# Optimization experiments

Measured on AMD Instinct MI355X. Metric: run time of the kernel, lower is better.

Reference implementation:

```python
import jax, jax.numpy as jnp
import numpy as np

P = 16          # patch size (square)
HEADS = 8
DH = 64         # dim per head
SCALE = DH ** -0.5
EPS = 1e-5


def layernorm(x, g, b):
    mu = x.mean(-1, keepdims=True)
    var = ((x - mu) ** 2).mean(-1, keepdims=True)
    return (x - mu) * jax.lax.rsqrt(var + EPS) * g + b


def sattn(q, k, v):
    # q:[..., i, d], k/v:[..., j, d]; q already scaled
    sim = jnp.einsum('...id,...jd->...ij', q, k)
    a = jax.nn.softmax(sim, axis=-1)
    return jnp.einsum('...ij,...jd->...id', a, v)


def split_heads(t, b, N):
    return t.reshape(b, N, HEADS, DH).transpose(0, 2, 1, 3).reshape(b * HEADS, N, DH)


def merge_heads(t, b, N):
    return t.reshape(b, HEADS, N, DH).transpose(0, 2, 1, 3).reshape(b, N, HEADS * DH)


def qkv_cls(x, ln_g, ln_b, qkv_w):
    b, N, _ = x.shape
    xn = layernorm(x, ln_g, ln_b)
    q, k, v = jnp.split(xn @ qkv_w, 3, axis=-1)
    q = split_heads(q, b, N) * SCALE
    k = split_heads(k, b, N)
    v = split_heads(v, b, N)
    cls_out = sattn(q[:, :1], k, v)          # cls attends to everything
    return q[:, 1:], k[:, 1:], v[:, 1:], k[:, :1], v[:, :1], cls_out


def time_attention(x, ln_g, ln_b, qkv_w, out_w, out_b, f, n):
    b, N, _ = x.shape
    q_, k_, v_, cls_k, cls_v, cls_out = qkv_cls(x, ln_g, ln_b, qkv_w)
    bh = b * HEADS
    resh = lambda t: t.reshape(bh, f, n, DH).transpose(0, 2, 1, 3)  # 'b (f n) d -> (b n) f d' kept as [bh,n,f,d]
    q_, k_, v_ = resh(q_), resh(k_), resh(v_)
    ck = jnp.broadcast_to(cls_k[:, None], (bh, n, 1, DH))
    cv = jnp.broadcast_to(cls_v[:, None], (bh, n, 1, DH))
    out = sattn(q_, jnp.concatenate([ck, k_], 2), jnp.concatenate([cv, v_], 2))
    out = out.transpose(0, 2, 1, 3).reshape(bh, f * n, DH)
    out = jnp.concatenate([cls_out, out], axis=1)
    return merge_heads(out, b, N) @ out_w + out_b


def space_attention(x, ln_g, ln_b, qkv_w, out_w, out_b, f, n):
    b, N, _ = x.shape
    q_, k_, v_, cls_k, cls_v, cls_out = qkv_cls(x, ln_g, ln_b, qkv_w)
    bh = b * HEADS
    resh = lambda t: t.reshape(bh, f, n, DH)  # 'b (f n) d -> (b f) n d' kept as [bh,f,n,d]
    q_, k_, v_ = resh(q_), resh(k_), resh(v_)
    m = n // 2
    ck = jnp.broadcast_to(cls_k[:, None], (bh, f, 1, DH))
    cv = jnp.broadcast_to(cls_v[:, None], (bh, f, 1, DH))
    # mutual attention: first half queries attend to [cls, second half], and vice versa
    out1 = sattn(q_[:, :, :m], jnp.concatenate([ck, k_[:, :, m:]], 2), jnp.concatenate([cv, v_[:, :, m:]], 2))
    out2 = sattn(q_[:, :, m:], jnp.concatenate([ck, k_[:, :, :m]], 2), jnp.concatenate([cv, v_[:, :, :m]], 2))
    out = jnp.concatenate([out1, out2], axis=2).reshape(bh, f * n, DH)
    out = jnp.concatenate([cls_out, out], axis=1)
    return merge_heads(out, b, N) @ out_w + out_b


def geglu_ff(x, ln_g, ln_b, w1, b1, w2, b2):
    xn = layernorm(x, ln_g, ln_b)
    h = xn @ w1 + b1
    u, g = jnp.split(h, 2, axis=-1)
    return (u * jax.nn.gelu(g, approximate=False)) @ w2 + b2


def setup_inputs() -> dict:
    key = jax.random.key(0)
    ks = jax.random.split(key, 12)
    D, DEPTH, NC = 512, 12, 60
    inner = HEADS * DH
    B, F, C, H, W = 1, 4, 3, 480, 640
    n = (H // P) * (W // P)        # 1200
    N = F * n + 1                  # 4801
    pd = C * P * P                 # 768
    s = 0.02
    rn = lambda k, sh: jax.random.normal(k, sh, jnp.float32) * s
    z = lambda sh: jnp.zeros(sh, jnp.float32)
    o = lambda sh: jnp.ones(sh, jnp.float32)
    return {
        'video': jax.random.normal(ks[0], (B, F, C, H, W), jnp.float32),
        'patch_w': rn(ks[1], (pd, D)), 'patch_b': z((D,)),
        'pos_emb': rn(ks[2], (N, D)),
        'cls_token': rn(ks[3], (1, D)),
        't_ln_g': o((DEPTH, D)), 't_ln_b': z((DEPTH, D)),
        't_qkv_w': rn(ks[4], (DEPTH, D, 3 * inner)),
        't_out_w': rn(ks[5], (DEPTH, inner, D)), 't_out_b': z((DEPTH, D)),
        's_ln_g': o((DEPTH, D)), 's_ln_b': z((DEPTH, D)),
        's_qkv_w': rn(ks[6], (DEPTH, D, 3 * inner)),
        's_out_w': rn(ks[7], (DEPTH, inner, D)), 's_out_b': z((DEPTH, D)),
        'f_ln_g': o((DEPTH, D)), 'f_ln_b': z((DEPTH, D)),
        'f_w1': rn(ks[8], (DEPTH, D, 8 * D)), 'f_b1': z((DEPTH, 8 * D)),
        'f_w2': rn(ks[9], (DEPTH, 4 * D, D)), 'f_b2': z((DEPTH, D)),
        'o_ln_g': o((D,)), 'o_ln_b': z((D,)),
        'o_w': rn(ks[10], (D, NC)), 'o_b': z((NC,)),
    }


def reference(video, patch_w, patch_b, pos_emb, cls_token,
              t_ln_g, t_ln_b, t_qkv_w, t_out_w, t_out_b,
              s_ln_g, s_ln_b, s_qkv_w, s_out_w, s_out_b,
              f_ln_g, f_ln_b, f_w1, f_b1, f_w2, f_b2,
              o_ln_g, o_ln_b, o_w, o_b):
    b, f, c, H, W = video.shape
    hh, ww = H // P, W // P
    n = hh * ww
    wh = ww // 2
    half = W // 2

    def patchify(v):  # v: [b,f,c,H,W/2] -> [b, f*hh*wh, P*P*c]
        v = v.reshape(b, f, c, hh, P, wh, P)
        v = v.transpose(0, 1, 3, 5, 4, 6, 2)  # b f h w p1 p2 c
        return v.reshape(b, f * hh * wh, P * P * c)

    tok = jnp.concatenate([patchify(video[..., :half]), patchify(video[..., half:])], axis=1)
    tok = tok @ patch_w + patch_b
    x = jnp.concatenate([jnp.broadcast_to(cls_token[None], (b, 1, tok.shape[-1])), tok], axis=1)
    x = x + pos_emb[: x.shape[1]]

    depth = t_qkv_w.shape[0]
    for i in range(depth):
        x = time_attention(x, t_ln_g[i], t_ln_b[i], t_qkv_w[i], t_out_w[i], t_out_b[i], f, n) + x
        x = space_attention(x, s_ln_g[i], s_ln_b[i], s_qkv_w[i], s_out_w[i], s_out_b[i], f, n) + x
        x = geglu_ff(x, f_ln_g[i], f_ln_b[i], f_w1[i], f_b1[i], f_w2[i], f_b2[i]) + x

    cls = layernorm(x[:, 0], o_ln_g, o_ln_b)
    return cls @ o_w + o_b
```

## Files before the change

kernel.cpp:

```cpp
#include <hip/hip_runtime.h>
#include <cmath>


#define NT      4801
#define NP      4800
#define MP      4864
#define DM      512
#define QKV_ST  1536
#define LN_EPS  1e-5f
#define NCH     49

typedef __attribute__((ext_vector_type(8))) short bf16x8;
typedef __attribute__((ext_vector_type(4))) float f32x4;

__device__ __forceinline__ unsigned short f2b(float f) {
    union { float f; unsigned int u; } x; x.f = f;
    unsigned int r = (x.u + 0x7FFFu + ((x.u >> 16) & 1u)) >> 16;
    return (unsigned short)r;
}
__device__ __forceinline__ float b2f(unsigned short b) {
    union { unsigned int u; float f; } x; x.u = ((unsigned int)b) << 16;
    return x.f;
}
__device__ __forceinline__ unsigned int pack2(float a, float b) {
    return (unsigned int)f2b(a) | ((unsigned int)f2b(b) << 16);
}

__device__ __forceinline__ void gl_lds16(const void* g, void* l) {
    __builtin_amdgcn_global_load_lds(
        (__attribute__((address_space(1))) unsigned int*)(unsigned long long)(uintptr_t)g,
        (__attribute__((address_space(3))) unsigned int*)l, 16, 0, 0);
}

__global__ void patchify_kernel(const float* __restrict__ video, unsigned short* __restrict__ out)
{
    int idx = blockIdx.x * 256 + threadIdx.x;
    if (idx >= NP * 768) return;
    int tok = idx / 768, e = idx % 768;
    int c  = e % 3;
    int pe = e / 3;
    int p2 = pe % 16, p1 = pe / 16;
    int half = tok / 2400, r = tok % 2400;
    int f = r / 600, rr = r % 600;
    int hi = rr / 20, wi = rr % 20;
    int row = hi * 16 + p1;
    int col = half * 320 + wi * 16 + p2;
    out[idx] = f2b(video[(((size_t)f * 3 + c) * 480 + row) * 640 + col]);
}

__global__ void cls_init_kernel(const float* __restrict__ cls_token,
                                const float* __restrict__ pos, float* __restrict__ X)
{
    int d = blockIdx.x * 256 + threadIdx.x;
    if (d < DM) X[d] = cls_token[d] + pos[d];
}

__device__ __forceinline__ void transpose_tile(const float* __restrict__ in,
                                               unsigned short* __restrict__ out,
                                               int K, int N, int tile)
{
    __shared__ float T[32][33];
    int ntk = K / 32;
    int kt = tile % ntk, nt = tile / ntk;
    int k0 = kt * 32, n0 = nt * 32;
    int tx = threadIdx.x & 31, ty = threadIdx.x >> 5;
    #pragma unroll
    for (int i = 0; i < 4; i++)
        T[ty + 8 * i][tx] = in[(size_t)(k0 + ty + 8 * i) * N + n0 + tx];
    __syncthreads();
    #pragma unroll
    for (int i = 0; i < 4; i++)
        out[(size_t)(n0 + ty + 8 * i) * K + k0 + tx] = f2b(T[tx][ty + 8 * i]);
}

__global__ __launch_bounds__(256) void convertT_layer(
    const float* __restrict__ w0, const float* __restrict__ w1,
    const float* __restrict__ w2, const float* __restrict__ w3,
    const float* __restrict__ w4, const float* __restrict__ w5,
    unsigned short* __restrict__ out)
{
    int t = blockIdx.x;
    if      (t <  768) transpose_tile(w0, out + 0,       512, 1536, t);
    else if (t < 1024) transpose_tile(w1, out + 786432,  512,  512, t - 768);
    else if (t < 1792) transpose_tile(w2, out + 1048576, 512, 1536, t - 1024);
    else if (t < 2048) transpose_tile(w3, out + 1835008, 512,  512, t - 1792);
    else if (t < 4096) transpose_tile(w4, out + 2097152, 512, 4096, t - 2048);
    else               transpose_tile(w5, out + 4194304, 2048, 512, t - 4096);
}

__global__ __launch_bounds__(256) void convertT_one(
    const float* __restrict__ in, unsigned short* __restrict__ out, int K, int N)
{
    transpose_tile(in, out, K, N, blockIdx.x);
}

template<bool OB16>
__global__ __launch_bounds__(256, 2) void mfma_gemm(
    const unsigned short* __restrict__ A, const unsigned short* __restrict__ BT,
    const float* __restrict__ bias, const float* __restrict__ add,
    void* __restrict__ C, int Mv, int N, int K)
{
    __shared__ short Asm[2][128 * 64];
    __shared__ short Bsm[2][128 * 64];
    const int tid = threadIdx.x, w = tid >> 6, lane = tid & 63;
    const int row0 = blockIdx.y * 128, col0 = blockIdx.x * 128;
    const int wm = w >> 1, wn = w & 1;
    const int l15 = lane & 15, quad = lane >> 4;

    f32x4 acc[4][4] = {};

    int arows[4], aqs[4];
    #pragma unroll
    for (int i = 0; i < 4; i++) {
        int s = (w * 4 + i) * 64 + lane;
        arows[i] = s >> 3;
        aqs[i]   = (s & 7) ^ ((s >> 3) & 7);
    }
    const unsigned short* Ab = A  + (size_t)row0 * K;
    const unsigned short* Bb = BT + (size_t)col0 * K;

    #pragma unroll
    for (int i = 0; i < 4; i++) {
        gl_lds16(Ab + (size_t)arows[i] * K + aqs[i] * 8, &Asm[0][(w * 4 + i) * 512]);
        gl_lds16(Bb + (size_t)arows[i] * K + aqs[i] * 8, &Bsm[0][(w * 4 + i) * 512]);
    }
    asm volatile("s_waitcnt vmcnt(0)" ::: "memory");
    __builtin_amdgcn_s_barrier();

    const int nt = K >> 6;
    int cur = 0;
    for (int t = 0; t < nt; t++) {
        if (t + 1 < nt) {
            const int k0 = (t + 1) << 6;
            #pragma unroll
            for (int i = 0; i < 4; i++) {
                gl_lds16(Ab + (size_t)arows[i] * K + k0 + aqs[i] * 8,
                         &Asm[cur ^ 1][(w * 4 + i) * 512]);
                gl_lds16(Bb + (size_t)arows[i] * K + k0 + aqs[i] * 8,
                         &Bsm[cur ^ 1][(w * 4 + i) * 512]);
            }
        }
        __builtin_amdgcn_sched_barrier(0);
        const short* As = Asm[cur];
        const short* Bs = Bsm[cur];
        #pragma unroll
        for (int ks = 0; ks < 2; ks++) {
            bf16x8 af[4], bfr[4];
            #pragma unroll
            for (int i = 0; i < 4; i++) {
                int m  = wm * 64 + i * 16 + l15;
                int pa = (ks * 4 + quad) ^ (m & 7);
                af[i]  = *(const bf16x8*)&As[m * 64 + pa * 8];
                int n  = wn * 64 + i * 16 + l15;
                int pb = (ks * 4 + quad) ^ (n & 7);
                bfr[i] = *(const bf16x8*)&Bs[n * 64 + pb * 8];
            }
            #pragma unroll
            for (int i = 0; i < 4; i++)
                #pragma unroll
                for (int j = 0; j < 4; j++)
                    acc[i][j] = __builtin_amdgcn_mfma_f32_16x16x32_bf16(
                                    af[i], bfr[j], acc[i][j], 0, 0, 0);
        }
        asm volatile("s_waitcnt vmcnt(0)" ::: "memory");
        __builtin_amdgcn_s_barrier();
        cur ^= 1;
    }

    #pragma unroll
    for (int i = 0; i < 4; i++) {
        #pragma unroll
        for (int r = 0; r < 4; r++) {
            int row = row0 + wm * 64 + i * 16 + quad * 4 + r;
            if (row >= Mv) continue;
            #pragma unroll
            for (int j = 0; j < 4; j++) {
                int col = col0 + wn * 64 + j * 16 + l15;
                float v = acc[i][j][r];
                if (bias) v += bias[col];
                if (add)  v += add[(size_t)row * N + col];
                if (OB16) ((unsigned short*)C)[(size_t)row * N + col] = f2b(v);
                else      ((float*)C)[(size_t)row * N + col] = v;
            }
        }
    }
}

template<int SPLITS>
__global__ __launch_bounds__(256, 2) void mfma_gemm_sk(
    const unsigned short* __restrict__ A, const unsigned short* __restrict__ BT,
    const float* __restrict__ bias, float* __restrict__ C, int Mv, int N, int K)
{
    __shared__ short Asm[2][128 * 64];
    __shared__ short Bsm[2][128 * 64];
    const int tid = threadIdx.x, w = tid >> 6, lane = tid & 63;
    const int row0 = blockIdx.y * 128, col0 = blockIdx.x * 128;
    const int wm = w >> 1, wn = w & 1;
    const int l15 = lane & 15, quad = lane >> 4;
    const int kchunk = K / SPLITS;
    const int kbeg = blockIdx.z * kchunk;

    f32x4 acc[4][4] = {};

    int arows[4], aqs[4];
    #pragma unroll
    for (int i = 0; i < 4; i++) {
        int s = (w * 4 + i) * 64 + lane;
        arows[i] = s >> 3;
        aqs[i]   = (s & 7) ^ ((s >> 3) & 7);
    }
    const unsigned short* Ab = A  + (size_t)row0 * K + kbeg;
    const unsigned short* Bb = BT + (size_t)col0 * K + kbeg;

    #pragma unroll
    for (int i = 0; i < 4; i++) {
        gl_lds16(Ab + (size_t)arows[i] * K + aqs[i] * 8, &Asm[0][(w * 4 + i) * 512]);
        gl_lds16(Bb + (size_t)arows[i] * K + aqs[i] * 8, &Bsm[0][(w * 4 + i) * 512]);
    }
    asm volatile("s_waitcnt vmcnt(0)" ::: "memory");
    __builtin_amdgcn_s_barrier();

    const int nt = kchunk >> 6;
    int cur = 0;
    for (int t = 0; t < nt; t++) {
        if (t + 1 < nt) {
            const int k0 = (t + 1) << 6;
            #pragma unroll
            for (int i = 0; i < 4; i++) {
                gl_lds16(Ab + (size_t)arows[i] * K + k0 + aqs[i] * 8,
                         &Asm[cur ^ 1][(w * 4 + i) * 512]);
                gl_lds16(Bb + (size_t)arows[i] * K + k0 + aqs[i] * 8,
                         &Bsm[cur ^ 1][(w * 4 + i) * 512]);
            }
        }
        __builtin_amdgcn_sched_barrier(0);
        const short* As = Asm[cur];
        const short* Bs = Bsm[cur];
        #pragma unroll
        for (int ks = 0; ks < 2; ks++) {
            bf16x8 af[4], bfr[4];
            #pragma unroll
            for (int i = 0; i < 4; i++) {
                int m  = wm * 64 + i * 16 + l15;
                int pa = (ks * 4 + quad) ^ (m & 7);
                af[i]  = *(const bf16x8*)&As[m * 64 + pa * 8];
                int n  = wn * 64 + i * 16 + l15;
                int pb = (ks * 4 + quad) ^ (n & 7);
                bfr[i] = *(const bf16x8*)&Bs[n * 64 + pb * 8];
            }
            #pragma unroll
            for (int i = 0; i < 4; i++)
                #pragma unroll
                for (int j = 0; j < 4; j++)
                    acc[i][j] = __builtin_amdgcn_mfma_f32_16x16x32_bf16(
                                    af[i], bfr[j], acc[i][j], 0, 0, 0);
        }
        asm volatile("s_waitcnt vmcnt(0)" ::: "memory");
        __builtin_amdgcn_s_barrier();
        cur ^= 1;
    }

    const bool addb = (blockIdx.z == 0) && (bias != nullptr);
    #pragma unroll
    for (int i = 0; i < 4; i++) {
        #pragma unroll
        for (int r = 0; r < 4; r++) {
            int row = row0 + wm * 64 + i * 16 + quad * 4 + r;
            if (row >= Mv) continue;
            #pragma unroll
            for (int j = 0; j < 4; j++) {
                int col = col0 + wn * 64 + j * 16 + l15;
                float v = acc[i][j][r];
                if (addb) v += bias[col];
                unsafeAtomicAdd(&C[(size_t)row * N + col], v);
            }
        }
    }
}

__global__ __launch_bounds__(256) void ln_bf16(
    const float* __restrict__ x, const float* __restrict__ g,
    const float* __restrict__ b, unsigned short* __restrict__ y, int M)
{
    int wid = threadIdx.x >> 6, lane = threadIdx.x & 63;
    int row = blockIdx.x * 4 + wid;
    if (row >= M) return;
    const float4* xr = (const float4*)(x + (size_t)row * DM);
    float4 v0 = xr[lane * 2], v1 = xr[lane * 2 + 1];
    float s  = v0.x + v0.y + v0.z + v0.w + v1.x + v1.y + v1.z + v1.w;
    float s2 = v0.x*v0.x + v0.y*v0.y + v0.z*v0.z + v0.w*v0.w
             + v1.x*v1.x + v1.y*v1.y + v1.z*v1.z + v1.w*v1.w;
    #pragma unroll
    for (int off = 32; off >= 1; off >>= 1) {
        s  += __shfl_xor(s, off);
        s2 += __shfl_xor(s2, off);
    }
    float mu = s * (1.f / DM);
    float var = s2 * (1.f / DM) - mu * mu;
    float r = rsqrtf(var + LN_EPS);
    const float4* gv = (const float4*)g;
    const float4* bv = (const float4*)b;
    unsigned int* yr = (unsigned int*)(y + (size_t)row * DM);
    #pragma unroll
    for (int i = 0; i < 2; i++) {
        float4 v = (i == 0) ? v0 : v1;
        float4 gg = gv[lane * 2 + i], bb = bv[lane * 2 + i];
        float ox = (v.x - mu) * r * gg.x + bb.x;
        float oy = (v.y - mu) * r * gg.y + bb.y;
        float oz = (v.z - mu) * r * gg.z + bb.z;
        float ow = (v.w - mu) * r * gg.w + bb.w;
        yr[lane * 4 + i * 2 + 0] = pack2(ox, oy);
        yr[lane * 4 + i * 2 + 1] = pack2(oz, ow);
    }
}

__global__ __launch_bounds__(256, 2) void time_attn(
    const unsigned short* __restrict__ qkv, unsigned short* __restrict__ out)
{
    int t = blockIdx.x * 256 + threadIdx.x;
    if (t >= 8 * NP) return;
    int h = t / NP, j = t - h * NP;
    int pos = j % 1200;
    union { bf16x8 v; unsigned short u[8]; } ld;
    float q[64];
    const unsigned short* qp = qkv + (size_t)(j + 1) * QKV_ST + h * 64;
    #pragma unroll
    for (int c = 0; c < 8; c++) {
        ld.v = *(const bf16x8*)(qp + c * 8);
        #pragma unroll
        for (int e = 0; e < 8; e++) q[c * 8 + e] = b2f(ld.u[e]) * 0.125f;
    }
    int rows[5] = {0, pos + 1, pos + 1201, pos + 2401, pos + 3601};
    float s[5];
    #pragma unroll
    for (int kk = 0; kk < 5; kk++) {
        const unsigned short* kp = qkv + (size_t)rows[kk] * QKV_ST + 512 + h * 64;
        float ss = 0.f;
        #pragma unroll
        for (int c = 0; c < 8; c++) {
            ld.v = *(const bf16x8*)(kp + c * 8);
            #pragma unroll
            for (int e = 0; e < 8; e++) ss += q[c * 8 + e] * b2f(ld.u[e]);
        }
        s[kk] = ss;
    }
    float mx = s[0];
    #pragma unroll
    for (int kk = 1; kk < 5; kk++) mx = fmaxf(mx, s[kk]);
    float e5[5], l = 0.f;
    #pragma unroll
    for (int kk = 0; kk < 5; kk++) { e5[kk] = __expf(s[kk] - mx); l += e5[kk]; }
    float rl = 1.f / l;
    float acc[64];
    #pragma unroll
    for (int d = 0; d < 64; d++) acc[d] = 0.f;
    #pragma unroll
    for (int kk = 0; kk < 5; kk++) {
        float p = e5[kk] * rl;
        const unsigned short* vp = qkv + (size_t)rows[kk] * QKV_ST + 1024 + h * 64;
        #pragma unroll
        for (int c = 0; c < 8; c++) {
            ld.v = *(const bf16x8*)(vp + c * 8);
            #pragma unroll
            for (int e = 0; e < 8; e++) acc[c * 8 + e] += p * b2f(ld.u[e]);
        }
    }
    unsigned int* op = (unsigned int*)(out + (size_t)(j + 1) * DM + h * 64);
    #pragma unroll
    for (int d2 = 0; d2 < 32; d2++) op[d2] = pack2(acc[2 * d2], acc[2 * d2 + 1]);
}

#define SPAD 72
__global__ __launch_bounds__(256, 2) void space_attn_mfma(
    const unsigned short* __restrict__ qkv, unsigned short* __restrict__ out)
{
    __shared__ short Ksm[64 * SPAD];
    __shared__ short VTsm[64 * SPAD];
    __shared__ short Psm[4][32 * SPAD];
    int qt = blockIdx.x, h = blockIdx.y, g = blockIdx.z;
    int f = g >> 1, half = g & 1;
    int tid = threadIdx.x, w = tid >> 6, lane = tid & 63;
    int l15 = lane & 15, quad = lane >> 4;

    int qrow_base = qt * 128 + w * 32;
    int qb = 1 + f * 1200 + half * 600;
    int kb = 1 + f * 1200 + (1 - half) * 600;

    bf16x8 aQ[2][2];
    #pragma unroll
    for (int mf = 0; mf < 2; mf++) {
        int qr = qrow_base + mf * 16 + l15;
        int qtok = qb + ((qr < 600) ? qr : 0);
        const unsigned short* qp = qkv + (size_t)qtok * QKV_ST + h * 64;
        #pragma unroll
        for (int ks = 0; ks < 2; ks++)
            aQ[mf][ks] = *(const bf16x8*)(qp + ks * 32 + quad * 8);
    }

    f32x4 O[2][4] = {};
    float mrow[2][4], lrow[2][4];
    #pragma unroll
    for (int mf = 0; mf < 2; mf++)
        #pragma unroll
        for (int r = 0; r < 4; r++) { mrow[mf][r] = -1e30f; lrow[mf][r] = 0.f; }

    for (int kt = 0; kt < 10; kt++) {
        __syncthreads();
        #pragma unroll
        for (int it = 0; it < 2; it++) {
            int c = tid + it * 256;
            int row = c >> 3, dc = (c & 7) * 8;
            int kidx = kt * 64 + row;
            int tok = (kidx == 0) ? 0 : ((kidx <= 600) ? kb + kidx - 1 : 0);
            const unsigned short* kp = qkv + (size_t)tok * QKV_ST + 512 + h * 64 + dc;
            *(bf16x8*)&Ksm[row * SPAD + dc] = *(const bf16x8*)kp;
            union { bf16x8 v; unsigned short u[8]; } vv;
            vv.v = *(const bf16x8*)(kp + 512);
            #pragma unroll
            for (int e = 0; e < 8; e++)
                VTsm[(dc + e) * SPAD + row] = vv.u[e];
        }
        __syncthreads();

        f32x4 S[2][4] = {};
        #pragma unroll
        for (int ks = 0; ks < 2; ks++) {
            bf16x8 bK[4];
            #pragma unroll
            for (int nf = 0; nf < 4; nf++)
                bK[nf] = *(const bf16x8*)&Ksm[(nf * 16 + l15) * SPAD + ks * 32 + quad * 8];
            #pragma unroll
            for (int mf = 0; mf < 2; mf++)
                #pragma unroll
                for (int nf = 0; nf < 4; nf++)
                    S[mf][nf] = __builtin_amdgcn_mfma_f32_16x16x32_bf16(
                                    aQ[mf][ks], bK[nf], S[mf][nf], 0, 0, 0);
        }

        #pragma unroll
        for (int mf = 0; mf < 2; mf++) {
            float pv[4][4];
            float lm[4] = {-1e30f, -1e30f, -1e30f, -1e30f};
            #pragma unroll
            for (int nf = 0; nf < 4; nf++) {
                int kidx = kt * 64 + nf * 16 + l15;
                bool valid = kidx <= 600;
                #pragma unroll
                for (int r = 0; r < 4; r++) {
                    float s = valid ? S[mf][nf][r] * 0.125f : -1e30f;
                    pv[nf][r] = s;
                    lm[r] = fmaxf(lm[r], s);
                }
            }
            #pragma unroll
            for (int off = 1; off < 16; off <<= 1)
                #pragma unroll
                for (int r = 0; r < 4; r++)
                    lm[r] = fmaxf(lm[r], __shfl_xor(lm[r], off));
            #pragma unroll
            for (int r = 0; r < 4; r++) {
                float nm = fmaxf(mrow[mf][r], lm[r]);
                float c = __expf(mrow[mf][r] - nm);
                mrow[mf][r] = nm;
                lrow[mf][r] *= c;
                #pragma unroll
                for (int nf = 0; nf < 4; nf++) O[mf][nf][r] *= c;
            }
            float rs[4] = {0.f, 0.f, 0.f, 0.f};
            #pragma unroll
            for (int nf = 0; nf < 4; nf++)
                #pragma unroll
                for (int r = 0; r < 4; r++) {
                    float p = __expf(pv[nf][r] - mrow[mf][r]);
                    pv[nf][r] = p;
                    rs[r] += p;
                }
            #pragma unroll
            for (int off = 1; off < 16; off <<= 1)
                #pragma unroll
                for (int r = 0; r < 4; r++)
                    rs[r] += __shfl_xor(rs[r], off);
            #pragma unroll
            for (int r = 0; r < 4; r++) lrow[mf][r] += rs[r];
            #pragma unroll
            for (int nf = 0; nf < 4; nf++)
                #pragma unroll
                for (int r = 0; r < 4; r++)
                    Psm[w][(mf * 16 + quad * 4 + r) * SPAD + nf * 16 + l15] = (short)f2b(pv[nf][r]);
        }
        asm volatile("s_waitcnt lgkmcnt(0)" ::: "memory");

        #pragma unroll
        for (int ks2 = 0; ks2 < 2; ks2++) {
            bf16x8 aP[2], bV[4];
            #pragma unroll
            for (int mf = 0; mf < 2; mf++)
                aP[mf] = *(const bf16x8*)&Psm[w][(mf * 16 + l15) * SPAD + ks2 * 32 + quad * 8];
            #pragma unroll
            for (int nf = 0; nf < 4; nf++)
                bV[nf] = *(const bf16x8*)&VTsm[(nf * 16 + l15) * SPAD + ks2 * 32 + quad * 8];
            #pragma unroll
            for (int mf = 0; mf < 2; mf++)
                #pragma unroll
                for (int nf = 0; nf < 4; nf++)
                    O[mf][nf] = __builtin_amdgcn_mfma_f32_16x16x32_bf16(
                                    aP[mf], bV[nf], O[mf][nf], 0, 0, 0);
        }
    }

    #pragma unroll
    for (int mf = 0; mf < 2; mf++)
        #pragma unroll
        for (int r = 0; r < 4; r++) {
            int qr = qrow_base + mf * 16 + quad * 4 + r;
            if (qr >= 600) continue;
            int qtok = qb + qr;
            float rl = 1.f / lrow[mf][r];
            #pragma unroll
            for (int nf = 0; nf < 4; nf++)
                out[(size_t)qtok * DM + h * 64 + nf * 16 + l15] = f2b(O[mf][nf][r] * rl);
        }
}

__global__ __launch_bounds__(256) void cls_attn_part(
    const unsigned short* __restrict__ qkv, float* __restrict__ part)
{
    int ch = blockIdx.x, h = blockIdx.y;
    int wid = threadIdx.x >> 6, lane = threadIdx.x & 63;
    __shared__ float sm[4], sl[4], sa[4][64];
    float qv = b2f(qkv[h * 64 + lane]) * 0.125f;
    int k0 = ch * 100 + wid * 25;
    float m = -1e30f, l = 0.f, acc = 0.f;
    for (int i = 0; i < 25; i += 2) {
        int key0 = k0 + i, key1 = key0 + 1;
        bool ok0 = key0 < NT;
        bool ok1 = (i + 1 < 25) && (key1 < NT);
        const unsigned short* kr0 = qkv + (size_t)(ok0 ? key0 : 0) * QKV_ST + 512 + h * 64;
        const unsigned short* kr1 = qkv + (size_t)(ok1 ? key1 : 0) * QKV_ST + 512 + h * 64;
        float s0 = qv * b2f(kr0[lane]);
        float v0 = b2f(kr0[512 + lane]);
        float s1 = qv * b2f(kr1[lane]);
        float v1 = b2f(kr1[512 + lane]);
        #pragma unroll
        for (int off = 32; off >= 1; off >>= 1) {
            s0 += __shfl_xor(s0, off);
            s1 += __shfl_xor(s1, off);
        }
        float nm = m;
        if (ok0) nm = fmaxf(nm, s0);
        if (ok1) nm = fmaxf(nm, s1);
        float c  = __expf(m - nm);
        float p0 = ok0 ? __expf(s0 - nm) : 0.f;
        float p1 = ok1 ? __expf(s1 - nm) : 0.f;
        l   = l * c + p0 + p1;
        acc = acc * c + p0 * v0 + p1 * v1;
        m = nm;
    }
    if (lane == 0) { sm[wid] = m; sl[wid] = l; }
    sa[wid][lane] = acc;
    __syncthreads();
    if (wid == 0) {
        float M2 = fmaxf(fmaxf(sm[0], sm[1]), fmaxf(sm[2], sm[3]));
        float L = 0.f, o = 0.f;
        #pragma unroll
        for (int w = 0; w < 4; w++) {
            float c = __expf(sm[w] - M2);
            L += sl[w] * c;
            o += sa[w][lane] * c;
        }
        float* p = part + ((size_t)h * NCH + ch) * 68;
        if (lane == 0) { p[0] = M2; p[1] = L; }
        p[4 + lane] = o;
    }
}

__global__ __launch_bounds__(64) void cls_attn_reduce(
    const float* __restrict__ part, unsigned short* __restrict__ out)
{
    int h = blockIdx.x, lane = threadIdx.x;
    float m = -1e30f, l = 0.f, acc = 0.f;
    for (int c = 0; c < NCH; c++) {
        const float* p = part + ((size_t)h * NCH + c) * 68;
        float cm = p[0], cl = p[1], ca = p[4 + lane];
        float nm = fmaxf(m, cm);
        float e1 = __expf(m - nm), e2 = __expf(cm - nm);
        l   = l * e1 + cl * e2;
        acc = acc * e1 + ca * e2;
        m = nm;
    }
    out[h * 64 + lane] = f2b(acc / l);
}

__global__ __launch_bounds__(256) void geglu_kernel(
    const unsigned short* __restrict__ h, unsigned short* __restrict__ out)
{
    int idx = blockIdx.x * 256 + threadIdx.x;
    if (idx >= NT * 256) return;
    int r = idx >> 8, cc = (idx & 255) * 8;
    const unsigned short* up = h + (size_t)r * 4096 + cc;
    const unsigned short* gp = up + 2048;
    float o[8];
    #pragma unroll
    for (int e = 0; e < 8; e++) {
        float u = b2f(up[e]), gg = b2f(gp[e]);
        o[e] = u * 0.5f * gg * (1.f + erff(gg * 0.70710678f));
    }
    unsigned int* op = (unsigned int*)(out + (size_t)r * 2048 + cc);
    #pragma unroll
    for (int e = 0; e < 4; e++) op[e] = pack2(o[2 * e], o[2 * e + 1]);
}

__global__ __launch_bounds__(64) void head_kernel(
    const float* __restrict__ x, const float* __restrict__ g,
    const float* __restrict__ b, const float* __restrict__ w,
    const float* __restrict__ ob, float* __restrict__ out)
{
    __shared__ float xn[DM];
    int lane = threadIdx.x;
    const float4* xr = (const float4*)x;
    float4 v0 = xr[lane * 2], v1 = xr[lane * 2 + 1];
    float s  = v0.x + v0.y + v0.z + v0.w + v1.x + v1.y + v1.z + v1.w;
    float s2 = v0.x*v0.x + v0.y*v0.y + v0.z*v0.z + v0.w*v0.w
             + v1.x*v1.x + v1.y*v1.y + v1.z*v1.z + v1.w*v1.w;
    #pragma unroll
    for (int off = 32; off >= 1; off >>= 1) {
        s  += __shfl_xor(s, off);
        s2 += __shfl_xor(s2, off);
    }
    float mu = s * (1.f / DM);
    float var = s2 * (1.f / DM) - mu * mu;
    float r = rsqrtf(var + LN_EPS);
    #pragma unroll
    for (int i = 0; i < 8; i++) {
        int d = lane * 8 + i;
        xn[d] = (x[d] - mu) * r * g[d] + b[d];
    }
    __syncthreads();
    if (lane < 60) {
        float a = ob[lane];
        for (int d = 0; d < DM; d++) a += xn[d] * w[d * 60 + lane];
        out[lane] = a;
    }
}

extern "C" void kernel_launch(void* const* d_in, const int* in_sizes, int n_in,
                              void* d_out, int out_size, void* d_ws, size_t ws_size,
                              hipStream_t stream)
{
    const float* video     = (const float*)d_in[0];
    const float* patch_w   = (const float*)d_in[1];
    const float* patch_b   = (const float*)d_in[2];
    const float* pos_emb   = (const float*)d_in[3];
    const float* cls_token = (const float*)d_in[4];
    const float* t_ln_g    = (const float*)d_in[5];
    const float* t_ln_b    = (const float*)d_in[6];
    const float* t_qkv_w   = (const float*)d_in[7];
    const float* t_out_w   = (const float*)d_in[8];
    const float* t_out_b   = (const float*)d_in[9];
    const float* s_ln_g    = (const float*)d_in[10];
    const float* s_ln_b    = (const float*)d_in[11];
    const float* s_qkv_w   = (const float*)d_in[12];
    const float* s_out_w   = (const float*)d_in[13];
    const float* s_out_b   = (const float*)d_in[14];
    const float* f_ln_g    = (const float*)d_in[15];
    const float* f_ln_b    = (const float*)d_in[16];
    const float* f_w1      = (const float*)d_in[17];
    const float* f_b1      = (const float*)d_in[18];
    const float* f_w2      = (const float*)d_in[19];
    const float* f_b2      = (const float*)d_in[20];
    const float* o_ln_g    = (const float*)d_in[21];
    const float* o_ln_b    = (const float*)d_in[22];
    const float* o_w       = (const float*)d_in[23];
    const float* o_b       = (const float*)d_in[24];

    char* ws = (char*)d_ws;
    size_t o = 0;
    float*          X    = (float*)(ws + o);          o += (size_t)(MP + 1) * 512 * 4;
    unsigned short* XN   = (unsigned short*)(ws + o); o += (size_t)MP * 512 * 2;
    unsigned short* QKV  = (unsigned short*)(ws + o); o += (size_t)MP * 1536 * 2;
    unsigned short* H16  = (unsigned short*)(ws + o); o += (size_t)MP * 4096 * 2;
    unsigned short* MID  = (unsigned short*)(ws + o); o += (size_t)MP * 2048 * 2;
    unsigned short* PT   = (unsigned short*)(ws + o); o += (size_t)MP * 768 * 2;
    unsigned short* W16  = (unsigned short*)(ws + o); o += (size_t)5242880 * 2;
    unsigned short* PW16 = (unsigned short*)(ws + o); o += (size_t)512 * 768 * 2;
    float*          CP   = (float*)(ws + o);          o += (size_t)8 * NCH * 68 * 4;

    patchify_kernel<<<(NP * 768 + 255) / 256, 256, 0, stream>>>(video, PT);
    cls_init_kernel<<<2, 256, 0, stream>>>(cls_token, pos_emb, X);
    convertT_one<<<(768 / 32) * (512 / 32), 256, 0, stream>>>(patch_w, PW16, 768, 512);
    mfma_gemm<false><<<dim3(4, 38), 256, 0, stream>>>(PT, PW16, patch_b, pos_emb + DM,
                                                      X + DM, NP, DM, 768);

    dim3 g_qkv(12, 38), g_ff1(32, 38);
    dim3 g_out_sk(4, 38, 2), g_ff2_sk(4, 38, 4);
    for (int i = 0; i < 12; i++) {
        convertT_layer<<<5120, 256, 0, stream>>>(
            t_qkv_w + (size_t)i * 512 * 1536, t_out_w + (size_t)i * 512 * 512,
            s_qkv_w + (size_t)i * 512 * 1536, s_out_w + (size_t)i * 512 * 512,
            f_w1 + (size_t)i * 512 * 4096, f_w2 + (size_t)i * 2048 * 512, W16);

        ln_bf16<<<1201, 256, 0, stream>>>(X, t_ln_g + i * DM, t_ln_b + i * DM, XN, NT);
        mfma_gemm<true><<<g_qkv, 256, 0, stream>>>(XN, W16 + 0, nullptr, nullptr,
                                                   QKV, NT, QKV_ST, DM);
        time_attn<<<150, 256, 0, stream>>>(QKV, MID);
        cls_attn_part<<<dim3(NCH, 8), 256, 0, stream>>>(QKV, CP);
        cls_attn_reduce<<<8, 64, 0, stream>>>(CP, MID);
        mfma_gemm_sk<2><<<g_out_sk, 256, 0, stream>>>(MID, W16 + 786432, t_out_b + i * DM,
                                                      X, NT, DM, DM);
        ln_bf16<<<1201, 256, 0, stream>>>(X, s_ln_g + i * DM, s_ln_b + i * DM, XN, NT);
        mfma_gemm<true><<<g_qkv, 256, 0, stream>>>(XN, W16 + 1048576, nullptr, nullptr,
                                                   QKV, NT, QKV_ST, DM);
        space_attn_mfma<<<dim3(5, 8, 8), 256, 0, stream>>>(QKV, MID);
        cls_attn_part<<<dim3(NCH, 8), 256, 0, stream>>>(QKV, CP);
        cls_attn_reduce<<<8, 64, 0, stream>>>(CP, MID);
        mfma_gemm_sk<2><<<g_out_sk, 256, 0, stream>>>(MID, W16 + 1835008, s_out_b + i * DM,
                                                      X, NT, DM, DM);
        ln_bf16<<<1201, 256, 0, stream>>>(X, f_ln_g + i * DM, f_ln_b + i * DM, XN, NT);
        mfma_gemm<true><<<g_ff1, 256, 0, stream>>>(XN, W16 + 2097152, f_b1 + i * 4096,
                                                   nullptr, H16, NT, 4096, DM);
        geglu_kernel<<<(NT * 256 + 255) / 256, 256, 0, stream>>>(H16, MID);
        mfma_gemm_sk<4><<<g_ff2_sk, 256, 0, stream>>>(MID, W16 + 4194304, f_b2 + i * DM,
                                                      X, NT, DM, 2048);
    }

    head_kernel<<<1, 64, 0, stream>>>(X, o_ln_g, o_ln_b, o_w, o_b, (float*)d_out);
}
```

Baseline: 4.653 ms.

## Fuse GEGLU into FF1 GEMM, remap blocks across XCDs, split time attention

```diff
diff --git a/kernel.cpp b/kernel.cpp
--- a/kernel.cpp
+++ b/kernel.cpp
@@ -30,6 +30,19 @@
     __builtin_amdgcn_global_load_lds(
         (__attribute__((address_space(1))) unsigned int*)(unsigned long long)(uintptr_t)g,
         (__attribute__((address_space(3))) unsigned int*)l, 16, 0, 0);
+}
+
+__device__ __forceinline__ void xcd_remap(int& bx, int& by, int& bz) {
+    const int gx = gridDim.x, gy = gridDim.y;
+    const int nwg = gx * gy * gridDim.z;
+    const int orig = (blockIdx.z * gy + blockIdx.y) * gx + blockIdx.x;
+    const int q = nwg >> 3, r = nwg & 7;
+    const int xcd = orig & 7, idx = orig >> 3;
+    const int id = (xcd < r ? xcd * (q + 1) : r * (q + 1) + (xcd - r) * q) + idx;
+    bx = id % gx;
+    const int t = id / gx;
+    by = t % gy;
+    bz = t / gy;
 }
 
 __global__ void patchify_kernel(const float* __restrict__ video, unsigned short* __restrict__ out)
@@ -55,6 +68,13 @@
     if (d < DM) X[d] = cls_token[d] + pos[d];
 }
 
+__global__ void posx_init(const float* __restrict__ pos, float* __restrict__ X)
+{
+    int i = blockIdx.x * 256 + threadIdx.x;
+    if (i < NP * DM / 4)
+        ((float4*)(X + DM))[i] = ((const float4*)(pos + DM))[i];
+}
+
 __device__ __forceinline__ void transpose_tile(const float* __restrict__ in,
                                                unsigned short* __restrict__ out,
                                                int K, int N, int tile)
@@ -102,30 +122,29 @@
 {
     __shared__ short Asm[2][128 * 64];
     __shared__ short Bsm[2][128 * 64];
+    int bx, by, bz; xcd_remap(bx, by, bz); (void)bz;
     const int tid = threadIdx.x, w = tid >> 6, lane = tid & 63;
-    const int row0 = blockIdx.y * 128, col0 = blockIdx.x * 128;
+    const int row0 = by * 128, col0 = bx * 128;
     const int wm = w >> 1, wn = w & 1;
     const int l15 = lane & 15, quad = lane >> 4;
 
     f32x4 acc[4][4] = {};
 
-    int arows[4], aqs[4];
+    int ar[4], aq[4];
     #pragma unroll
     for (int i = 0; i < 4; i++) {
-        int s = (w * 4 + i) * 64 + lane;
-        arows[i] = s >> 3;
-        aqs[i]   = (s & 7) ^ ((s >> 3) & 7);
+        int c = (w * 4 + i) * 64 + lane;
+        ar[i] = c >> 3;
+        aq[i] = (c & 7) ^ ((c >> 3) & 7);
     }
     const unsigned short* Ab = A  + (size_t)row0 * K;
     const unsigned short* Bb = BT + (size_t)col0 * K;
 
     #pragma unroll
     for (int i = 0; i < 4; i++) {
-        gl_lds16(Ab + (size_t)arows[i] * K + aqs[i] * 8, &Asm[0][(w * 4 + i) * 512]);
-        gl_lds16(Bb + (size_t)arows[i] * K + aqs[i] * 8, &Bsm[0][(w * 4 + i) * 512]);
-    }
-    asm volatile("s_waitcnt vmcnt(0)" ::: "memory");
-    __builtin_amdgcn_s_barrier();
+        gl_lds16(Ab + (size_t)ar[i] * K + aq[i] * 8, &Asm[0][(w * 4 + i) * 512]);
+        gl_lds16(Bb + (size_t)ar[i] * K + aq[i] * 8, &Bsm[0][(w * 4 + i) * 512]);
+    }
 
     const int nt = K >> 6;
     int cur = 0;
@@ -134,13 +153,15 @@
             const int k0 = (t + 1) << 6;
             #pragma unroll
             for (int i = 0; i < 4; i++) {
-                gl_lds16(Ab + (size_t)arows[i] * K + k0 + aqs[i] * 8,
+                gl_lds16(Ab + (size_t)ar[i] * K + k0 + aq[i] * 8,
                          &Asm[cur ^ 1][(w * 4 + i) * 512]);
-                gl_lds16(Bb + (size_t)arows[i] * K + k0 + aqs[i] * 8,
+                gl_lds16(Bb + (size_t)ar[i] * K + k0 + aq[i] * 8,
                          &Bsm[cur ^ 1][(w * 4 + i) * 512]);
             }
-        }
-        __builtin_amdgcn_sched_barrier(0);
+            asm volatile("s_waitcnt vmcnt(8)\ns_barrier" ::: "memory");
+        } else {
+            asm volatile("s_waitcnt vmcnt(0)\ns_barrier" ::: "memory");
+        }
         const short* As = Asm[cur];
         const short* Bs = Bsm[cur];
         #pragma unroll
@@ -149,11 +170,9 @@
             #pragma unroll
             for (int i = 0; i < 4; i++) {
                 int m  = wm * 64 + i * 16 + l15;
-                int pa = (ks * 4 + quad) ^ (m & 7);
-                af[i]  = *(const bf16x8*)&As[m * 64 + pa * 8];
+                af[i]  = *(const bf16x8*)&As[m * 64 + (((ks * 4 + quad) ^ (m & 7))) * 8];
                 int n  = wn * 64 + i * 16 + l15;
-                int pb = (ks * 4 + quad) ^ (n & 7);
-                bfr[i] = *(const bf16x8*)&Bs[n * 64 + pb * 8];
+                bfr[i] = *(const bf16x8*)&Bs[n * 64 + (((ks * 4 + quad) ^ (n & 7))) * 8];
             }
             #pragma unroll
             for (int i = 0; i < 4; i++)
@@ -162,8 +181,7 @@
                     acc[i][j] = __builtin_amdgcn_mfma_f32_16x16x32_bf16(
                                     af[i], bfr[j], acc[i][j], 0, 0, 0);
         }
-        asm volatile("s_waitcnt vmcnt(0)" ::: "memory");
-        __builtin_amdgcn_s_barrier();
+        asm volatile("s_barrier" ::: "memory");
         cur ^= 1;
     }
 
@@ -193,32 +211,31 @@
 {
     __shared__ short Asm[2][128 * 64];
     __shared__ short Bsm[2][128 * 64];
+    int bx, by, bz; xcd_remap(bx, by, bz);
     const int tid = threadIdx.x, w = tid >> 6, lane = tid & 63;
-    const int row0 = blockIdx.y * 128, col0 = blockIdx.x * 128;
+    const int row0 = by * 128, col0 = bx * 128;
     const int wm = w >> 1, wn = w & 1;
     const int l15 = lane & 15, quad = lane >> 4;
     const int kchunk = K / SPLITS;
-    const int kbeg = blockIdx.z * kchunk;
+    const int kbeg = bz * kchunk;
 
     f32x4 acc[4][4] = {};
 
-    int arows[4], aqs[4];
+    int ar[4], aq[4];
     #pragma unroll
     for (int i = 0; i < 4; i++) {
-        int s = (w * 4 + i) * 64 + lane;
-        arows[i] = s >> 3;
-        aqs[i]   = (s & 7) ^ ((s >> 3) & 7);
+        int c = (w * 4 + i) * 64 + lane;
+        ar[i] = c >> 3;
+        aq[i] = (c & 7) ^ ((c >> 3) & 7);
     }
     const unsigned short* Ab = A  + (size_t)row0 * K + kbeg;
     const unsigned short* Bb = BT + (size_t)col0 * K + kbeg;
 
     #pragma unroll
     for (int i = 0; i < 4; i++) {
-        gl_lds16(Ab + (size_t)arows[i] * K + aqs[i] * 8, &Asm[0][(w * 4 + i) * 512]);
-        gl_lds16(Bb + (size_t)arows[i] * K + aqs[i] * 8, &Bsm[0][(w * 4 + i) * 512]);
-    }
-    asm volatile("s_waitcnt vmcnt(0)" ::: "memory");
-    __builtin_amdgcn_s_barrier();
+        gl_lds16(Ab + (size_t)ar[i] * K + aq[i] * 8, &Asm[0][(w * 4 + i) * 512]);
+        gl_lds16(Bb + (size_t)ar[i] * K + aq[i] * 8, &Bsm[0][(w * 4 + i) * 512]);
+    }
 
     const int nt = kchunk >> 6;
     int cur = 0;
@@ -227,13 +244,15 @@
             const int k0 = (t + 1) << 6;
             #pragma unroll
             for (int i = 0; i < 4; i++) {
-                gl_lds16(Ab + (size_t)arows[i] * K + k0 + aqs[i] * 8,
+                gl_lds16(Ab + (size_t)ar[i] * K + k0 + aq[i] * 8,
                          &Asm[cur ^ 1][(w * 4 + i) * 512]);
-                gl_lds16(Bb + (size_t)arows[i] * K + k0 + aqs[i] * 8,
+                gl_lds16(Bb + (size_t)ar[i] * K + k0 + aq[i] * 8,
                          &Bsm[cur ^ 1][(w * 4 + i) * 512]);
             }
-        }
-        __builtin_amdgcn_sched_barrier(0);
+            asm volatile("s_waitcnt vmcnt(8)\ns_barrier" ::: "memory");
+        } else {
+            asm volatile("s_waitcnt vmcnt(0)\ns_barrier" ::: "memory");
+        }
         const short* As = Asm[cur];
         const short* Bs = Bsm[cur];
         #pragma unroll
@@ -242,11 +261,9 @@
             #pragma unroll
             for (int i = 0; i < 4; i++) {
                 int m  = wm * 64 + i * 16 + l15;
-                int pa = (ks * 4 + quad) ^ (m & 7);
-                af[i]  = *(const bf16x8*)&As[m * 64 + pa * 8];
+                af[i]  = *(const bf16x8*)&As[m * 64 + (((ks * 4 + quad) ^ (m & 7))) * 8];
                 int n  = wn * 64 + i * 16 + l15;
-                int pb = (ks * 4 + quad) ^ (n & 7);
-                bfr[i] = *(const bf16x8*)&Bs[n * 64 + pb * 8];
+                bfr[i] = *(const bf16x8*)&Bs[n * 64 + (((ks * 4 + quad) ^ (n & 7))) * 8];
             }
             #pragma unroll
             for (int i = 0; i < 4; i++)
@@ -255,12 +272,11 @@
                     acc[i][j] = __builtin_amdgcn_mfma_f32_16x16x32_bf16(
                                     af[i], bfr[j], acc[i][j], 0, 0, 0);
         }
-        asm volatile("s_waitcnt vmcnt(0)" ::: "memory");
-        __builtin_amdgcn_s_barrier();
+        asm volatile("s_barrier" ::: "memory");
         cur ^= 1;
     }
 
-    const bool addb = (blockIdx.z == 0) && (bias != nullptr);
+    const bool addb = (bz == 0) && (bias != nullptr);
     #pragma unroll
     for (int i = 0; i < 4; i++) {
         #pragma unroll
@@ -273,6 +289,85 @@
                 float v = acc[i][j][r];
                 if (addb) v += bias[col];
                 unsafeAtomicAdd(&C[(size_t)row * N + col], v);
+            }
+        }
+    }
+}
+
+__global__ __launch_bounds__(256, 2) void mfma_ff1_geglu(
+    const unsigned short* __restrict__ A, const unsigned short* __restrict__ BT,
+    const float* __restrict__ b1, unsigned short* __restrict__ out, int Mv)
+{
+    __shared__ short Asm[128 * 64];
+    __shared__ short Bu[128 * 64];
+    __shared__ short Bg[128 * 64];
+    int bx, by, bz; xcd_remap(bx, by, bz); (void)bz;
+    const int tid = threadIdx.x, w = tid >> 6, lane = tid & 63;
+    const int row0 = by * 128, colu0 = bx * 128;
+    const int wm = w >> 1, wn = w & 1;
+    const int l15 = lane & 15, quad = lane >> 4;
+
+    f32x4 au[4][4] = {};
+    f32x4 ag[4][4] = {};
+
+    int ar[4], aq[4];
+    #pragma unroll
+    for (int i = 0; i < 4; i++) {
+        int c = (w * 4 + i) * 64 + lane;
+        ar[i] = c >> 3;
+        aq[i] = (c & 7) ^ ((c >> 3) & 7);
+    }
+    const unsigned short* Ab  = A  + (size_t)row0 * 512;
+    const unsigned short* Bub = BT + (size_t)colu0 * 512;
+    const unsigned short* Bgb = BT + (size_t)(colu0 + 2048) * 512;
+
+    for (int k0 = 0; k0 < 512; k0 += 64) {
+        #pragma unroll
+        for (int i = 0; i < 4; i++) {
+            gl_lds16(Ab  + (size_t)ar[i] * 512 + k0 + aq[i] * 8, &Asm[(w * 4 + i) * 512]);
+            gl_lds16(Bub + (size_t)ar[i] * 512 + k0 + aq[i] * 8, &Bu[(w * 4 + i) * 512]);
+            gl_lds16(Bgb + (size_t)ar[i] * 512 + k0 + aq[i] * 8, &Bg[(w * 4 + i) * 512]);
+        }
+        __syncthreads();
+        #pragma unroll
+        for (int ks = 0; ks < 2; ks++) {
+            bf16x8 af[4], bu[4], bg[4];
+            #pragma unroll
+            for (int i = 0; i < 4; i++) {
+                int m = wm * 64 + i * 16 + l15;
+                int p = (((ks * 4 + quad) ^ (m & 7))) * 8;
+                af[i] = *(const bf16x8*)&Asm[m * 64 + p];
+                int n = wn * 64 + i * 16 + l15;
+                int pb = (((ks * 4 + quad) ^ (n & 7))) * 8;
+                bu[i] = *(const bf16x8*)&Bu[n * 64 + pb];
+                bg[i] = *(const bf16x8*)&Bg[n * 64 + pb];
+            }
+            #pragma unroll
+            for (int i = 0; i < 4; i++)
+                #pragma unroll
+                for (int j = 0; j < 4; j++) {
+                    au[i][j] = __builtin_amdgcn_mfma_f32_16x16x32_bf16(
+                                   af[i], bu[j], au[i][j], 0, 0, 0);
+                    ag[i][j] = __builtin_amdgcn_mfma_f32_16x16x32_bf16(
+                                   af[i], bg[j], ag[i][j], 0, 0, 0);
+                }
+        }
+        __syncthreads();
+    }
+
+    #pragma unroll
+    for (int i = 0; i < 4; i++) {
+        #pragma unroll
+        for (int r = 0; r < 4; r++) {
+            int row = row0 + wm * 64 + i * 16 + quad * 4 + r;
+            if (row >= Mv) continue;
+            #pragma unroll
+            for (int j = 0; j < 4; j++) {
+                int col = colu0 + wn * 64 + j * 16 + l15;
+                float u = au[i][j][r] + b1[col];
+                float g = ag[i][j][r] + b1[col + 2048];
+                float h = u * 0.5f * g * (1.f + erff(g * 0.70710678f));
+                out[(size_t)row * 2048 + col] = f2b(h);
             }
         }
     }
@@ -314,18 +409,21 @@
     }
 }
 
-__global__ __launch_bounds__(256, 2) void time_attn(
+__global__ __launch_bounds__(256, 4) void time_attn4(
     const unsigned short* __restrict__ qkv, unsigned short* __restrict__ out)
 {
-    int t = blockIdx.x * 256 + threadIdx.x;
-    if (t >= 8 * NP) return;
-    int h = t / NP, j = t - h * NP;
+    int tid = threadIdx.x;
+    int dq = tid & 3, tl = tid >> 2;
+    int b = blockIdx.x;
+    int h = b / 75;
+    int j = (b - h * 75) * 64 + tl;
     int pos = j % 1200;
+    int d0 = dq * 16;
     union { bf16x8 v; unsigned short u[8]; } ld;
-    float q[64];
-    const unsigned short* qp = qkv + (size_t)(j + 1) * QKV_ST + h * 64;
-    #pragma unroll
-    for (int c = 0; c < 8; c++) {
+    float q[16];
+    const unsigned short* qp = qkv + (size_t)(j + 1) * QKV_ST + h * 64 + d0;
+    #pragma unroll
+    for (int c = 0; c < 2; c++) {
         ld.v = *(const bf16x8*)(qp + c * 8);
         #pragma unroll
         for (int e = 0; e < 8; e++) q[c * 8 + e] = b2f(ld.u[e]) * 0.125f;
@@ -334,14 +432,16 @@
     float s[5];
     #pragma unroll
     for (int kk = 0; kk < 5; kk++) {
-        const unsigned short* kp = qkv + (size_t)rows[kk] * QKV_ST + 512 + h * 64;
+        const unsigned short* kp = qkv + (size_t)rows[kk] * QKV_ST + 512 + h * 64 + d0;
         float ss = 0.f;
         #pragma unroll
-        for (int c = 0; c < 8; c++) {
+        for (int c = 0; c < 2; c++) {
             ld.v = *(const bf16x8*)(kp + c * 8);
             #pragma unroll
             for (int e = 0; e < 8; e++) ss += q[c * 8 + e] * b2f(ld.u[e]);
         }
+        ss += __shfl_xor(ss, 1);
+        ss += __shfl_xor(ss, 2);
         s[kk] = ss;
     }
     float mx = s[0];
@@ -351,23 +451,23 @@
     #pragma unroll
     for (int kk = 0; kk < 5; kk++) { e5[kk] = __expf(s[kk] - mx); l += e5[kk]; }
     float rl = 1.f / l;
-    float acc[64];
-    #pragma unroll
-    for (int d = 0; d < 64; d++) acc[d] = 0.f;
+    float acc[16];
+    #pragma unroll
+    for (int d = 0; d < 16; d++) acc[d] = 0.f;
     #pragma unroll
     for (int kk = 0; kk < 5; kk++) {
         float p = e5[kk] * rl;
-        const unsigned short* vp = qkv + (size_t)rows[kk] * QKV_ST + 1024 + h * 64;
-        #pragma unroll
-        for (int c = 0; c < 8; c++) {
+        const unsigned short* vp = qkv + (size_t)rows[kk] * QKV_ST + 1024 + h * 64 + d0;
+        #pragma unroll
+        for (int c = 0; c < 2; c++) {
             ld.v = *(const bf16x8*)(vp + c * 8);
             #pragma unroll
             for (int e = 0; e < 8; e++) acc[c * 8 + e] += p * b2f(ld.u[e]);
         }
     }
-    unsigned int* op = (unsigned int*)(out + (size_t)(j + 1) * DM + h * 64);
-    #pragma unroll
-    for (int d2 = 0; d2 < 32; d2++) op[d2] = pack2(acc[2 * d2], acc[2 * d2 + 1]);
+    unsigned int* op = (unsigned int*)(out + (size_t)(j + 1) * DM + h * 64 + d0);
+    #pragma unroll
+    for (int d2 = 0; d2 < 8; d2++) op[d2] = pack2(acc[2 * d2], acc[2 * d2 + 1]);
 }
 
 #define SPAD 72
@@ -589,25 +689,6 @@
         m = nm;
     }
     out[h * 64 + lane] = f2b(acc / l);
-}
-
-__global__ __launch_bounds__(256) void geglu_kernel(
-    const unsigned short* __restrict__ h, unsigned short* __restrict__ out)
-{
-    int idx = blockIdx.x * 256 + threadIdx.x;
-    if (idx >= NT * 256) return;
-    int r = idx >> 8, cc = (idx & 255) * 8;
-    const unsigned short* up = h + (size_t)r * 4096 + cc;
-    const unsigned short* gp = up + 2048;
-    float o[8];
-    #pragma unroll
-    for (int e = 0; e < 8; e++) {
-        float u = b2f(up[e]), gg = b2f(gp[e]);
-        o[e] = u * 0.5f * gg * (1.f + erff(gg * 0.70710678f));
-    }
-    unsigned int* op = (unsigned int*)(out + (size_t)r * 2048 + cc);
-    #pragma unroll
-    for (int e = 0; e < 4; e++) op[e] = pack2(o[2 * e], o[2 * e + 1]);
 }
 
 __global__ __launch_bounds__(64) void head_kernel(
@@ -687,11 +768,12 @@
 
     patchify_kernel<<<(NP * 768 + 255) / 256, 256, 0, stream>>>(video, PT);
     cls_init_kernel<<<2, 256, 0, stream>>>(cls_token, pos_emb, X);
+    posx_init<<<NP * DM / 4 / 256, 256, 0, stream>>>(pos_emb, X);
     convertT_one<<<(768 / 32) * (512 / 32), 256, 0, stream>>>(patch_w, PW16, 768, 512);
-    mfma_gemm<false><<<dim3(4, 38), 256, 0, stream>>>(PT, PW16, patch_b, pos_emb + DM,
-                                                      X + DM, NP, DM, 768);
-
-    dim3 g_qkv(12, 38), g_ff1(32, 38);
+    mfma_gemm_sk<3><<<dim3(4, 38, 3), 256, 0, stream>>>(PT, PW16, patch_b,
+                                                        X + DM, NP, DM, 768);
+
+    dim3 g_qkv(12, 38), g_ff1(16, 38);
     dim3 g_out_sk(4, 38, 2), g_ff2_sk(4, 38, 4);
     for (int i = 0; i < 12; i++) {
         convertT_layer<<<5120, 256, 0, stream>>>(
@@ -702,7 +784,7 @@
         ln_bf16<<<1201, 256, 0, stream>>>(X, t_ln_g + i * DM, t_ln_b + i * DM, XN, NT);
         mfma_gemm<true><<<g_qkv, 256, 0, stream>>>(XN, W16 + 0, nullptr, nullptr,
                                                    QKV, NT, QKV_ST, DM);
-        time_attn<<<150, 256, 0, stream>>>(QKV, MID);
+        time_attn4<<<600, 256, 0, stream>>>(QKV, MID);
         cls_attn_part<<<dim3(NCH, 8), 256, 0, stream>>>(QKV, CP);
         cls_attn_reduce<<<8, 64, 0, stream>>>(CP, MID);
         mfma_gemm_sk<2><<<g_out_sk, 256, 0, stream>>>(MID, W16 + 786432, t_out_b + i * DM,
@@ -716,9 +798,8 @@
         mfma_gemm_sk<2><<<g_out_sk, 256, 0, stream>>>(MID, W16 + 1835008, s_out_b + i * DM,
                                                       X, NT, DM, DM);
         ln_bf16<<<1201, 256, 0, stream>>>(X, f_ln_g + i * DM, f_ln_b + i * DM, XN, NT);
-        mfma_gemm<true><<<g_ff1, 256, 0, stream>>>(XN, W16 + 2097152, f_b1 + i * 4096,
-                                                   nullptr, H16, NT, 4096, DM);
-        geglu_kernel<<<(NT * 256 + 255) / 256, 256, 0, stream>>>(H16, MID);
+        mfma_ff1_geglu<<<g_ff1, 256, 0, stream>>>(XN, W16 + 2097152, f_b1 + i * 4096,
+                                                  MID, NT);
         mfma_gemm_sk<4><<<g_ff2_sk, 256, 0, stream>>>(MID, W16 + 4194304, f_b2 + i * DM,
                                                       X, NT, DM, 2048);
     }
```

Measured after the change: 4.383 ms. 5.8% less time.
